# Optimization experiments

Measured on AMD Instinct MI355X. Metric: run time of the kernel, lower is better.

## Reference

```python
import jax, jax.numpy as jnp
import numpy as np

B = 8
S = 512  # seq_len


def setup_inputs() -> dict:
    key = jax.random.key(0)
    kx, kw, kb = jax.random.split(key, 3)
    x = jax.random.normal(kx, (B, S, S), dtype=jnp.float32)
    # Padded block of per-diagonal Linear weights: W[i, k, j] is weight[k, j]
    # of nn.Linear(i+1, i+1); entries with k > i or j > i are zero.
    i_d = jnp.arange(S)[:, None, None]
    k_d = jnp.arange(S)[None, :, None]
    j_d = jnp.arange(S)[None, None, :]
    wmask = ((k_d <= i_d) & (j_d <= i_d)).astype(jnp.float32)
    W = jax.random.normal(kw, (S, S, S), dtype=jnp.float32) * 0.02 * wmask
    bmask = (jnp.arange(S)[None, :] <= jnp.arange(S)[:, None]).astype(jnp.float32)
    b = jax.random.normal(kb, (S, S), dtype=jnp.float32) * 0.02 * bmask
    return {"x": x, "W": W, "b": b}


def reference(x, W, b):
    # For each anti-diagonal i (positions (r, i-r), r=0..i, with r+c=i<S):
    #   gather d = x[:, r, i-r], apply Linear_i: out = d @ W_i^T + b_i,
    #   scatter back reversed: x[:, r, i-r] = out[i-r]  =>  x[b,r,c]=out[b,r+c,c].
    S_ = x.shape[-1]
    i_idx = jnp.arange(S_)[:, None]   # diagonal index
    r_idx = jnp.arange(S_)[None, :]   # position along diagonal
    cols = (i_idx - r_idx) % S_
    valid = (r_idx <= i_idx)[None]                       # [1,S,S]
    # D[b, i, r] = x[b, r, i-r] for r<=i else 0
    D = jnp.where(valid, x[:, r_idx, cols], 0.0)         # [B,S,S]
    # Batched per-diagonal matmul: out[b,i,k] = sum_j W[i,k,j] D[b,i,j] + b[i,k]
    out = jnp.einsum('bij,ikj->bik', D, W) + b[None]     # [B,S,S]
    # Scatter back with reversal: x[b,r,c] = out[b, r+c, c] when r+c < S
    rr = jnp.arange(S_)[:, None]
    cc = jnp.arange(S_)[None, :]
    diag = rr + cc
    ok = (diag < S_)[None]
    new_x = jnp.where(ok, out[:, jnp.minimum(diag, S_ - 1), cc], x)
    return new_x
```

## Files before the change

kernel.cpp:

```cpp
#include <hip/hip_runtime.h>

#define S 512
#define NB 8
#define KT 256
#define JT 32

__global__ __launch_bounds__(256) void tail_copy_kernel(const float* __restrict__ x,
                                                        float* __restrict__ out) {
  int idx = blockIdx.x * 256 + threadIdx.x;
  int c = idx & (S - 1);
  int r = (idx >> 9) & (S - 1);
  if (r + c >= S) out[idx] = x[idx];
}

__global__ __launch_bounds__(256, 3) void diag_linear_kernel(const float* __restrict__ x,
                                                             const float* __restrict__ W,
                                                             const float* __restrict__ bias,
                                                             float* __restrict__ out) {
  __shared__ __align__(16) float WtBuf[JT * KT];
  __shared__ __align__(16) float DlBuf[S * NB];

  const int i  = (S - 1) - (int)blockIdx.x;
  const int k0 = (int)blockIdx.y * KT;
  if (k0 > i) return;

  const int tid  = threadIdx.x;
  const int wave = tid >> 6;
  const int lane = tid & 63;

  const int jend = (i + JT) & ~(JT - 1);

  for (int idx = tid; idx < jend * NB; idx += 256) {
    const int j = idx >> 3;
    const int b = idx & 7;
    DlBuf[idx] = (j <= i) ? x[b * (S * S) + j * S + (i - j)] : 0.0f;
  }

  float acc[4][NB];
#pragma unroll
  for (int m = 0; m < 4; ++m)
#pragma unroll
    for (int b = 0; b < NB; ++b) acc[m][b] = 0.0f;

  const int  k       = k0 + tid;
  const bool krow_ok = (k <= i);
  const float* wrow  = W + ((size_t)i * S + k) * S;

  float4 v[8];
#pragma unroll
  for (int q = 0; q < 8; ++q)
    v[q] = krow_ok ? *(const float4*)(wrow + 4 * q)
                   : make_float4(0.f, 0.f, 0.f, 0.f);

  for (int j0 = 0; j0 < jend; j0 += JT) {
    __syncthreads();
#pragma unroll
    for (int q = 0; q < 8; ++q) {
      WtBuf[(4 * q + 0) * KT + tid] = v[q].x;
      WtBuf[(4 * q + 1) * KT + tid] = v[q].y;
      WtBuf[(4 * q + 2) * KT + tid] = v[q].z;
      WtBuf[(4 * q + 3) * KT + tid] = v[q].w;
    }
    const int jn = j0 + JT;
    if (jn < jend && krow_ok) {
#pragma unroll
      for (int q = 0; q < 8; ++q)
        v[q] = *(const float4*)(wrow + jn + 4 * q);
    }
    __syncthreads();

#pragma unroll
    for (int u = 0; u < 8; ++u) {
      const int jl = (wave << 3) + u;
      const float4 wv = *(const float4*)&WtBuf[jl * KT + (lane << 2)];
      const float4 dA = *(const float4*)&DlBuf[(j0 + jl) * NB];
      const float4 dB = *(const float4*)&DlBuf[(j0 + jl) * NB + 4];
      const float wm[4] = {wv.x, wv.y, wv.z, wv.w};
#pragma unroll
      for (int m = 0; m < 4; ++m) {
        acc[m][0] = fmaf(wm[m], dA.x, acc[m][0]);
        acc[m][1] = fmaf(wm[m], dA.y, acc[m][1]);
        acc[m][2] = fmaf(wm[m], dA.z, acc[m][2]);
        acc[m][3] = fmaf(wm[m], dA.w, acc[m][3]);
        acc[m][4] = fmaf(wm[m], dB.x, acc[m][4]);
        acc[m][5] = fmaf(wm[m], dB.y, acc[m][5]);
        acc[m][6] = fmaf(wm[m], dB.z, acc[m][6]);
        acc[m][7] = fmaf(wm[m], dB.w, acc[m][7]);
      }
    }
  }

  __syncthreads();
  float* Racc = WtBuf;

  for (int w = 0; w < 4; ++w) {
    if (wave == w) {
#pragma unroll
      for (int b = 0; b < NB; ++b) {
        float4* p = (float4*)&Racc[b * KT + (lane << 2)];
        float4 cur = make_float4(acc[0][b], acc[1][b], acc[2][b], acc[3][b]);
        if (w != 0) {
          float4 old = *p;
          cur.x += old.x; cur.y += old.y; cur.z += old.z; cur.w += old.w;
        }
        *p = cur;
      }
    }
    __syncthreads();
  }

  if (krow_ok) {
    const float bv = bias[i * S + k];
    const int r = i - k;
#pragma unroll
    for (int b = 0; b < NB; ++b)
      out[b * (S * S) + r * S + k] = Racc[b * KT + tid] + bv;
  }
}

extern "C" void kernel_launch(void* const* d_in, const int* in_sizes, int n_in,
                              void* d_out, int out_size, void* d_ws, size_t ws_size,
                              hipStream_t stream) {
  const float* x    = (const float*)d_in[0];
  const float* W    = (const float*)d_in[1];
  const float* bias = (const float*)d_in[2];
  float* out = (float*)d_out;

  (void)d_ws; (void)ws_size; (void)in_sizes; (void)n_in; (void)out_size;

  tail_copy_kernel<<<dim3((NB * S * S) / 256), 256, 0, stream>>>(x, out);
  diag_linear_kernel<<<dim3(S, 2), 256, 0, stream>>>(x, W, bias, out);
}
```

Baseline: 653.4 us.

## Coalesce W tile loads, swizzle shared-memory transpose, and remap diagonal order

W tiles are now loaded so that eight consecutive threads read 128 contiguous bytes of one row, in place of each thread streaming its own row. The goal is coalesced global access. The transpose into shared memory uses an XOR swizzle to avoid bank conflicts on the scattered stores, and reads apply the matching swizzle. Block indices are also permuted so diagonals of different lengths are interleaved across XCDs to balance the triangular workload. The added index arithmetic and the swizzle could cost some extra ALU work.

```diff
diff --git a/kernel.cpp b/kernel.cpp
--- a/kernel.cpp
+++ b/kernel.cpp
@@ -20,7 +20,10 @@
   __shared__ __align__(16) float WtBuf[JT * KT];
   __shared__ __align__(16) float DlBuf[S * NB];
 
-  const int i  = (S - 1) - (int)blockIdx.x;
+  const int bx = (int)blockIdx.x;
+  const int u  = bx >> 3;
+  const int xc = bx & 7;
+  const int i  = (S - 1) - ((u & 15) + 16 * (xc + 8 * (u >> 4)));
   const int k0 = (int)blockIdx.y * KT;
   if (k0 > i) return;
 
@@ -42,37 +45,45 @@
 #pragma unroll
     for (int b = 0; b < NB; ++b) acc[m][b] = 0.0f;
 
-  const int  k       = k0 + tid;
-  const bool krow_ok = (k <= i);
-  const float* wrow  = W + ((size_t)i * S + k) * S;
+  const int kl_base = tid >> 3;
+  const int jb      = (tid & 7) << 2;
+  const float* Wdiag = W + (size_t)i * S * S;
 
   float4 v[8];
-#pragma unroll
-  for (int q = 0; q < 8; ++q)
-    v[q] = krow_ok ? *(const float4*)(wrow + 4 * q)
-                   : make_float4(0.f, 0.f, 0.f, 0.f);
+#define LOAD_TILE(J0)                                                          \
+  {                                                                            \
+    _Pragma("unroll")                                                          \
+    for (int p = 0; p < 8; ++p) {                                              \
+      const int k = k0 + (p << 5) + kl_base;                                   \
+      v[p] = (k <= i) ? *(const float4*)(Wdiag + (size_t)k * S + (J0) + jb)    \
+                      : make_float4(0.f, 0.f, 0.f, 0.f);                       \
+    }                                                                          \
+  }
+
+  LOAD_TILE(0)
 
   for (int j0 = 0; j0 < jend; j0 += JT) {
     __syncthreads();
 #pragma unroll
-    for (int q = 0; q < 8; ++q) {
-      WtBuf[(4 * q + 0) * KT + tid] = v[q].x;
-      WtBuf[(4 * q + 1) * KT + tid] = v[q].y;
-      WtBuf[(4 * q + 2) * KT + tid] = v[q].z;
-      WtBuf[(4 * q + 3) * KT + tid] = v[q].w;
+    for (int p = 0; p < 8; ++p) {
+      const int kl = (p << 5) + kl_base;
+      const int c  = kl >> 2;
+      const int w  = kl & 3;
+      const float e[4] = {v[p].x, v[p].y, v[p].z, v[p].w};
+#pragma unroll
+      for (int q = 0; q < 4; ++q) {
+        const int j = jb + q;
+        WtBuf[j * KT + (((c ^ (j & 7)) << 2) | w)] = e[q];
+      }
     }
     const int jn = j0 + JT;
-    if (jn < jend && krow_ok) {
-#pragma unroll
-      for (int q = 0; q < 8; ++q)
-        v[q] = *(const float4*)(wrow + jn + 4 * q);
-    }
+    if (jn < jend) LOAD_TILE(jn)
     __syncthreads();
 
 #pragma unroll
-    for (int u = 0; u < 8; ++u) {
-      const int jl = (wave << 3) + u;
-      const float4 wv = *(const float4*)&WtBuf[jl * KT + (lane << 2)];
+    for (int uu = 0; uu < 8; ++uu) {
+      const int jl = (wave << 3) + uu;
+      const float4 wv = *(const float4*)&WtBuf[jl * KT + ((lane ^ (jl & 7)) << 2)];
       const float4 dA = *(const float4*)&DlBuf[(j0 + jl) * NB];
       const float4 dB = *(const float4*)&DlBuf[(j0 + jl) * NB + 4];
       const float wm[4] = {wv.x, wv.y, wv.z, wv.w};
@@ -109,7 +120,8 @@
     __syncthreads();
   }
 
-  if (krow_ok) {
+  const int k = k0 + tid;
+  if (k <= i) {
     const float bv = bias[i * S + k];
     const int r = i - k;
 #pragma unroll
```

Result: slower. 828.9 us (+26.9%).

## Prefetch W tiles two steps ahead and remap diagonals across XCDs

Applied to the files above, without the earlier changes.

Replaces the single register prefetch buffer with two register groups, so weight tiles are loaded two JT-steps ahead of the shared-memory stage. The goal is to hide more global-load latency in this latency-bound triangular matvec. It also permutes blockIdx.x into diagonal indices so that blocks landing on each of the 8 XCDs take interleaved 16-diagonal chunks, which should balance the triangular work. The trade-off is more registers per thread. Indexing v[t&1] at runtime may also force scratch memory if the compiler does not resolve it, which would hurt occupancy or add memory traffic.

```diff
diff --git a/kernel.cpp b/kernel.cpp
--- a/kernel.cpp
+++ b/kernel.cpp
@@ -20,7 +20,10 @@
   __shared__ __align__(16) float WtBuf[JT * KT];
   __shared__ __align__(16) float DlBuf[S * NB];
 
-  const int i  = (S - 1) - (int)blockIdx.x;
+  const int bx = (int)blockIdx.x;
+  const int u  = bx >> 3;
+  const int xc = bx & 7;
+  const int i  = (S - 1) - ((u & 15) + 16 * (xc + 8 * (u >> 4)));
   const int k0 = (int)blockIdx.y * KT;
   if (k0 > i) return;
 
@@ -29,6 +32,7 @@
   const int lane = tid & 63;
 
   const int jend = (i + JT) & ~(JT - 1);
+  const int T    = jend >> 5;
 
   for (int idx = tid; idx < jend * NB; idx += 256) {
     const int j = idx >> 3;
@@ -46,32 +50,45 @@
   const bool krow_ok = (k <= i);
   const float* wrow  = W + ((size_t)i * S + k) * S;
 
-  float4 v[8];
+  float4 v[2][8];
+  if (!krow_ok) {
 #pragma unroll
-  for (int q = 0; q < 8; ++q)
-    v[q] = krow_ok ? *(const float4*)(wrow + 4 * q)
-                   : make_float4(0.f, 0.f, 0.f, 0.f);
+    for (int g = 0; g < 2; ++g)
+#pragma unroll
+      for (int q = 0; q < 8; ++q) v[g][q] = make_float4(0.f, 0.f, 0.f, 0.f);
+  }
 
-  for (int j0 = 0; j0 < jend; j0 += JT) {
+#define LOAD_GRP(g, J0)                                                        \
+  if (krow_ok) {                                                               \
+    _Pragma("unroll")                                                          \
+    for (int q = 0; q < 8; ++q)                                                \
+      v[g][q] = *(const float4*)(wrow + (J0) + 4 * q);                         \
+  }
+
+  LOAD_GRP(0, 0)
+  if (T > 1) LOAD_GRP(1, 32)
+
+  for (int t = 0; t < T; ++t) {
+    const int pb = t & 1;
+    const int j0 = t << 5;
     __syncthreads();
+    {
+      const float4* vv = v[pb];
 #pragma unroll
-    for (int q = 0; q < 8; ++q) {
-      WtBuf[(4 * q + 0) * KT + tid] = v[q].x;
-      WtBuf[(4 * q + 1) * KT + tid] = v[q].y;
-      WtBuf[(4 * q + 2) * KT + tid] = v[q].z;
-      WtBuf[(4 * q + 3) * KT + tid] = v[q].w;
+      for (int q = 0; q < 8; ++q) {
+        WtBuf[(4 * q + 0) * KT + tid] = vv[q].x;
+        WtBuf[(4 * q + 1) * KT + tid] = vv[q].y;
+        WtBuf[(4 * q + 2) * KT + tid] = vv[q].z;
+        WtBuf[(4 * q + 3) * KT + tid] = vv[q].w;
+      }
     }
-    const int jn = j0 + JT;
-    if (jn < jend && krow_ok) {
-#pragma unroll
-      for (int q = 0; q < 8; ++q)
-        v[q] = *(const float4*)(wrow + jn + 4 * q);
-    }
+    const int tn = t + 2;
+    if (tn < T) LOAD_GRP(pb, tn << 5)
     __syncthreads();
 
 #pragma unroll
-    for (int u = 0; u < 8; ++u) {
-      const int jl = (wave << 3) + u;
+    for (int uu = 0; uu < 8; ++uu) {
+      const int jl = (wave << 3) + uu;
       const float4 wv = *(const float4*)&WtBuf[jl * KT + (lane << 2)];
       const float4 dA = *(const float4*)&DlBuf[(j0 + jl) * NB];
       const float4 dB = *(const float4*)&DlBuf[(j0 + jl) * NB + 4];
```

New measurement: 716.9 us. 1.1x slower.
